# Kernel tuning notes

Hardware: AMD Instinct MI355X
Metric: run time of the kernel (lower is better)

The kernel has to match this reference:

```python
import jax, jax.numpy as jnp
import numpy as np

HIDDEN = 512
B, H, W = 8, 48, 48
SCALE = 1.0 / np.sqrt(HIDDEN).astype(np.float32)


def conv1x1(x, w, b):
    # x: [B, C, H, W], w: [O, C], b: [O]  (1x1 Conv2d == channel matmul)
    return jnp.einsum('bchw,oc->bohw', x, w) + b[None, :, None, None]


def setup_inputs() -> dict:
    key = jax.random.key(0)
    ks = jax.random.split(key, 10)
    s = 1.0 / np.sqrt(HIDDEN)
    return {
        'locx': jax.random.normal(ks[0], (B, HIDDEN, H, W), dtype=jnp.float32),
        'glox': jax.random.normal(ks[1], (B, HIDDEN, H, W), dtype=jnp.float32),
        'Wq': jax.random.normal(ks[2], (HIDDEN, HIDDEN), dtype=jnp.float32) * s,
        'bq': jax.random.normal(ks[3], (HIDDEN,), dtype=jnp.float32) * 0.01,
        'Wk': jax.random.normal(ks[4], (HIDDEN, HIDDEN), dtype=jnp.float32) * s,
        'bk': jax.random.normal(ks[5], (HIDDEN,), dtype=jnp.float32) * 0.01,
        'Wv': jax.random.normal(ks[6], (HIDDEN, HIDDEN), dtype=jnp.float32) * s,
        'bv': jax.random.normal(ks[7], (HIDDEN,), dtype=jnp.float32) * 0.01,
        'Wo': jax.random.normal(ks[8], (HIDDEN, HIDDEN), dtype=jnp.float32) * s,
        'bo': jax.random.normal(ks[9], (HIDDEN,), dtype=jnp.float32) * 0.01,
    }


def reference(locx, glox, Wq, bq, Wk, bk, Wv, bv, Wo, bo):
    b, c, h, w = locx.shape
    # 1x1 conv projections
    q = conv1x1(locx, Wq, bq).reshape(b, c, h * w)   # [B, C, N]
    k = conv1x1(glox, Wk, bk).reshape(b, c, -1)      # [B, C, M]
    v = conv1x1(glox, Wv, bv).reshape(b, c, -1)      # [B, C, M]
    # scores = Q^T K / sqrt(hidden)  -> [B, N, M]
    scores = jnp.einsum('bcn,bcm->bnm', q, k) * SCALE
    probs = jax.nn.softmax(scores, axis=-1)           # dropout rate 0.0 -> identity
    # context = probs @ V^T -> [B, N, C] -> [B, C, H, H]
    ctx = jnp.einsum('bnm,bcm->bcn', probs, v).reshape(b, c, h, h)
    out = conv1x1(ctx, Wo, bo)                        # proj dropout 0.0 -> identity
    return out
```

## Files before the change

kernel.cpp:

```cpp
#include <hip/hip_runtime.h>
#include <hip/hip_bf16.h>

typedef __attribute__((ext_vector_type(4))) float f32x4;
typedef __attribute__((ext_vector_type(8))) short bf16x8;
typedef __attribute__((ext_vector_type(4))) short s16x4;

#define C_DIM 512
#define N_PIX 2304
#define N_BATCH 8
#define ATT_SCALE 0.04419417382415922f
#define NJB 18

typedef __attribute__((address_space(3))) unsigned int lds_u32;
typedef const __attribute__((address_space(1))) unsigned int glob_u32;

__device__ __forceinline__ void gl2lds16(const __hip_bfloat16* g, __hip_bfloat16* l)
{
    __builtin_amdgcn_global_load_lds((glob_u32*)g, (lds_u32*)l, 16, 0, 0);
}

template<int OUT_BF16, int BIAS_MODE, int EPI>
__global__ __launch_bounds__(256)
void gemm_bt(const __hip_bfloat16* __restrict__ A, const __hip_bfloat16* __restrict__ B,
             void* __restrict__ Dp, const float* __restrict__ bias,
             float* __restrict__ rsum,
             float scale, int K, int lda, int ldb, int ldd,
             long sA, long sB, long sD)
{
    __shared__ __hip_bfloat16 As[128 * 64];
    __shared__ __hip_bfloat16 Bs[128 * 64];

    const int tid  = threadIdx.x;
    const int lane = tid & 63;
    const int wave = tid >> 6;
    const int i0 = blockIdx.x * 128;
    const int j0 = blockIdx.y * 128;
    const size_t bz = blockIdx.z;

    const __hip_bfloat16* Ab = A + bz * (size_t)sA;
    const __hip_bfloat16* Bb = B + bz * (size_t)sB;
    __hip_bfloat16* D16 = (__hip_bfloat16*)Dp + bz * (size_t)sD;
    float*          D32 = (float*)Dp          + bz * (size_t)sD;

    const int lrow = lane >> 3;
    const int lcs  = (lane & 7) ^ lrow;
    const __hip_bfloat16* ga = Ab + (size_t)(i0 + wave * 32 + lrow) * lda + lcs * 8;
    const __hip_bfloat16* gb = Bb + (size_t)(j0 + wave * 32 + lrow) * ldb + lcs * 8;
    __hip_bfloat16* la = As + wave * 32 * 64;
    __hip_bfloat16* lb = Bs + wave * 32 * 64;

    const int fr = lane & 15;
    const int fq = lane >> 4;
    const int sw = fr & 7;
    const int wi = (wave >> 1) * 64;
    const int wj = (wave & 1) * 64;

    f32x4 acc[4][4];
#pragma unroll
    for (int a = 0; a < 4; ++a)
#pragma unroll
        for (int b = 0; b < 4; ++b)
            acc[a][b] = (f32x4){0.f, 0.f, 0.f, 0.f};

    for (int k0 = 0; k0 < K; k0 += 64) {
#pragma unroll
        for (int s = 0; s < 4; ++s) {
            gl2lds16(ga + (size_t)s * 8 * lda + k0, la + s * 8 * 64);
            gl2lds16(gb + (size_t)s * 8 * ldb + k0, lb + s * 8 * 64);
        }
        __syncthreads();

#pragma unroll
        for (int kk = 0; kk < 2; ++kk) {
            bf16x8 af[4], bfr[4];
            const int ca = ((kk * 4 + fq) ^ sw) << 3;
#pragma unroll
            for (int t = 0; t < 4; ++t) {
                af[t]  = *(const bf16x8*)(&As[(wi + t * 16 + fr) * 64 + ca]);
                bfr[t] = *(const bf16x8*)(&Bs[(wj + t * 16 + fr) * 64 + ca]);
            }
#pragma unroll
            for (int a = 0; a < 4; ++a)
#pragma unroll
                for (int b = 0; b < 4; ++b)
                    acc[a][b] = __builtin_amdgcn_mfma_f32_16x16x32_bf16(
                        af[a], bfr[b], acc[a][b], 0, 0, 0);
        }
        __syncthreads();
    }

    const int orow = fq * 4;

    float inv[4][4];
    if (EPI == 2) {
        const float* ri = rsum + bz * N_PIX;
#pragma unroll
        for (int a = 0; a < 4; ++a)
#pragma unroll
            for (int r = 0; r < 4; ++r)
                inv[a][r] = ri[i0 + wi + a * 16 + orow + r];
    }

    float rpart[4][4];
    if (EPI == 1) {
#pragma unroll
        for (int a = 0; a < 4; ++a)
#pragma unroll
            for (int r = 0; r < 4; ++r)
                rpart[a][r] = 0.f;
    }

#pragma unroll
    for (int a = 0; a < 4; ++a) {
        int ib = i0 + wi + a * 16 + orow;
#pragma unroll
        for (int b = 0; b < 4; ++b) {
            int j = j0 + wj + b * 16 + fr;
            float bj = (BIAS_MODE == 2) ? bias[j] : 0.f;
#pragma unroll
            for (int r = 0; r < 4; ++r) {
                int i = ib + r;
                float v = acc[a][b][r] * scale;
                if (BIAS_MODE == 1) v += bias[i];
                if (BIAS_MODE == 2) v += bj;
                if (EPI == 1) { v = __expf(v); rpart[a][r] += v; }
                if (EPI == 2) v *= inv[a][r];
                if (OUT_BF16)
                    D16[(size_t)i * ldd + j] = __float2bfloat16(v);
                else
                    D32[(size_t)i * ldd + j] = v;
            }
        }
    }

    if (EPI == 1) {
#pragma unroll
        for (int m = 1; m < 16; m <<= 1)
#pragma unroll
            for (int a = 0; a < 4; ++a)
#pragma unroll
                for (int r = 0; r < 4; ++r)
                    rpart[a][r] += __shfl_xor(rpart[a][r], m);
        float* rsl = (float*)As;
        if (fr == 0) {
#pragma unroll
            for (int a = 0; a < 4; ++a)
#pragma unroll
                for (int r = 0; r < 4; ++r)
                    rsl[wave * 64 + a * 16 + orow + r] = rpart[a][r];
        }
        __syncthreads();
        if (tid < 128) {
            int half = tid >> 6, rr = tid & 63;
            float s = rsl[(half * 2) * 64 + rr] + rsl[(half * 2 + 1) * 64 + rr];
            rsum[((size_t)blockIdx.y * N_BATCH + bz) * N_PIX + i0 + tid] = s;
        }
    }
}

__global__ __launch_bounds__(256)
void reduce_rinv(const float* __restrict__ rp, float* __restrict__ rinv)
{
    int idx = blockIdx.x * 256 + threadIdx.x;
    float s = 0.f;
#pragma unroll
    for (int jb = 0; jb < NJB; ++jb)
        s += rp[(size_t)jb * N_BATCH * N_PIX + idx];
    rinv[idx] = 1.f / s;
}

__global__ __launch_bounds__(256)
void transpose_cast(const float* __restrict__ X, __hip_bfloat16* __restrict__ Xt)
{
    __shared__ float t[64 * 65];
    const int n0 = blockIdx.x * 64;
    const int c0 = blockIdx.y * 64;
    const size_t b = blockIdx.z;
    const float* Xb = X + b * (size_t)C_DIM * N_PIX;
    const int tid = threadIdx.x;

    const int n_l = tid & 63;
    const int c_b = tid >> 6;
#pragma unroll
    for (int s = 0; s < 16; ++s) {
        int c_l = c_b + s * 4;
        t[c_l * 65 + n_l] = Xb[(size_t)(c0 + c_l) * N_PIX + n0 + n_l];
    }
    __syncthreads();

    const int cc = (tid & 7) * 8;
    const int nb = tid >> 3;
#pragma unroll
    for (int it = 0; it < 2; ++it) {
        int n2 = nb + it * 32;
        union { __hip_bfloat16 h[8]; int4 v; } u;
#pragma unroll
        for (int w = 0; w < 8; ++w)
            u.h[w] = __float2bfloat16(t[(cc + w) * 65 + n2]);
        *(int4*)(&Xt[((size_t)b * N_PIX + n0 + n2) * C_DIM + c0 + cc]) = u.v;
    }
}

__global__ __launch_bounds__(256)
void cast_w4(const float* __restrict__ s0, const float* __restrict__ s1,
             const float* __restrict__ s2, const float* __restrict__ s3,
             __hip_bfloat16* __restrict__ dst)
{
    const float* srcs[4] = {s0, s1, s2, s3};
    const int w = blockIdx.y;
    const int i = (blockIdx.x * 256 + threadIdx.x) * 4;
    float4 f = *(const float4*)(srcs[w] + i);
    union { __hip_bfloat16 h[4]; s16x4 q; } t;
    t.h[0] = __float2bfloat16(f.x);
    t.h[1] = __float2bfloat16(f.y);
    t.h[2] = __float2bfloat16(f.z);
    t.h[3] = __float2bfloat16(f.w);
    *(s16x4*)(dst + (size_t)w * C_DIM * C_DIM + i) = t.q;
}

extern "C" void kernel_launch(void* const* d_in, const int* in_sizes, int n_in,
                              void* d_out, int out_size, void* d_ws, size_t ws_size,
                              hipStream_t stream)
{
    const float* locx = (const float*)d_in[0];
    const float* glox = (const float*)d_in[1];
    const float* Wq = (const float*)d_in[2];
    const float* bq = (const float*)d_in[3];
    const float* Wk = (const float*)d_in[4];
    const float* bk = (const float*)d_in[5];
    const float* Wv = (const float*)d_in[6];
    const float* bv = (const float*)d_in[7];
    const float* Wo = (const float*)d_in[8];
    const float* bo = (const float*)d_in[9];
    float* out = (float*)d_out;

    const int C = C_DIM, N = N_PIX;
    const size_t WB   = (size_t)C * C * 2;
    const size_t szX  = (size_t)N_BATCH * N * C * 2;
    const size_t szP1 = (size_t)N * N * 2;
    const size_t szRP = (size_t)NJB * N_BATCH * N * 4;
    const size_t szRI = (size_t)N_BATCH * N * 4;

    const size_t fixed = 4 * WB + 6 * szX + szRP + szRI;
    int nb = 1;
    for (int cand : {8, 4, 2, 1})
        if (ws_size >= fixed + (size_t)cand * szP1 + 8 * 256) { nb = cand; break; }

    char* ws = (char*)d_ws;
    size_t off = 0;
    auto alloc = [&](size_t bytes) {
        char* p = ws + off;
        off += (bytes + 255) & ~(size_t)255;
        return p;
    };
    __hip_bfloat16* wgt = (__hip_bfloat16*)alloc(4 * WB);
    __hip_bfloat16* Xl  = (__hip_bfloat16*)alloc(szX);
    __hip_bfloat16* Xg  = (__hip_bfloat16*)alloc(szX);
    __hip_bfloat16* Qt  = (__hip_bfloat16*)alloc(szX);
    __hip_bfloat16* Kt  = (__hip_bfloat16*)alloc(szX);
    __hip_bfloat16* Vb  = (__hip_bfloat16*)alloc(szX);
    __hip_bfloat16* Ctx = (__hip_bfloat16*)alloc(szX);
    float*          rp   = (float*)alloc(szRP);
    float*          rinv = (float*)alloc(szRI);
    __hip_bfloat16* Pu  = (__hip_bfloat16*)alloc((size_t)nb * szP1);

    __hip_bfloat16* wq_b = wgt;
    __hip_bfloat16* wk_b = wgt + (size_t)C * C;
    __hip_bfloat16* wv_b = wgt + 2 * (size_t)C * C;
    __hip_bfloat16* wo_b = wgt + 3 * (size_t)C * C;

    const dim3 blk(256);
    const long sPr = (long)N * C;
    const long sV  = (long)C * N;

    cast_w4<<<dim3(C * C / 1024, 4), blk, 0, stream>>>(Wq, Wk, Wv, Wo, wgt);
    transpose_cast<<<dim3(N / 64, C / 64, 8), blk, 0, stream>>>(locx, Xl);
    transpose_cast<<<dim3(N / 64, C / 64, 8), blk, 0, stream>>>(glox, Xg);

    gemm_bt<1, 2, 0><<<dim3(N / 128, C / 128, 8), blk, 0, stream>>>(
        Xl, wq_b, Qt, bq, nullptr, 1.f, C, C, C, C, sPr, 0, sPr);
    gemm_bt<1, 2, 0><<<dim3(N / 128, C / 128, 8), blk, 0, stream>>>(
        Xg, wk_b, Kt, bk, nullptr, 1.f, C, C, C, C, sPr, 0, sPr);
    gemm_bt<1, 1, 0><<<dim3(C / 128, N / 128, 8), blk, 0, stream>>>(
        wv_b, Xg, Vb, bv, nullptr, 1.f, C, C, C, N, 0, sPr, sV);

    for (int r = 0; r < N_BATCH; r += nb) {
        gemm_bt<1, 0, 1><<<dim3(N / 128, N / 128, nb), blk, 0, stream>>>(
            Qt + (size_t)r * sPr, Kt + (size_t)r * sPr, Pu, nullptr,
            rp + (size_t)r * N, ATT_SCALE, C, C, C, N, sPr, sPr, (long)N * N);
        reduce_rinv<<<dim3(nb * N / 256), blk, 0, stream>>>(
            rp + (size_t)r * N, rinv + (size_t)r * N);
        gemm_bt<1, 0, 2><<<dim3(N / 128, C / 128, nb), blk, 0, stream>>>(
            Pu, Vb + (size_t)r * sV, Ctx + (size_t)r * sPr, nullptr,
            rinv + (size_t)r * N, 1.f, N, N, N, C, (long)N * N, sV, sPr);
    }

    gemm_bt<0, 1, 0><<<dim3(C / 128, N / 128, 8), blk, 0, stream>>>(
        wo_b, Ctx, out, bo, nullptr, 1.f, C, C, C, N, 0, sPr, sV);
}
```

Before: 390.6 us.

## Remap GEMM grid to batch-fastest 1D order and merge Q/K projections

Replaces the 3D grid with a 1D launch in which the batch index varies fastest, so consecutive workgroups share the same weight tile and reuse it from cache. The Q and K projection GEMMs are merged into one launch that selects operand pointers per block, cutting one kernel launch and raising occupancy on the small projection grids. The workspace fallback is simplified to either all batches at once or one batch at a time. This adds per-block index arithmetic and branching.

```diff
diff --git a/kernel.cpp b/kernel.cpp
--- a/kernel.cpp
+++ b/kernel.cpp
@@ -19,28 +19,41 @@
     __builtin_amdgcn_global_load_lds((glob_u32*)g, (lds_u32*)l, 16, 0, 0);
 }
 
-template<int OUT_BF16, int BIAS_MODE, int EPI>
+template<int OUT_BF16, int BIAS_MODE, int EPI, int MERGE2, int NJ, int NS>
 __global__ __launch_bounds__(256)
-void gemm_bt(const __hip_bfloat16* __restrict__ A, const __hip_bfloat16* __restrict__ B,
-             void* __restrict__ Dp, const float* __restrict__ bias,
+void gemm_bt(const __hip_bfloat16* __restrict__ A0, const __hip_bfloat16* __restrict__ B0,
+             void* __restrict__ D0, const float* __restrict__ bias0,
              float* __restrict__ rsum,
+             const __hip_bfloat16* __restrict__ A1, const __hip_bfloat16* __restrict__ B1,
+             void* __restrict__ D1, const float* __restrict__ bias1,
              float scale, int K, int lda, int ldb, int ldd,
              long sA, long sB, long sD)
 {
     __shared__ __hip_bfloat16 As[128 * 64];
     __shared__ __hip_bfloat16 Bs[128 * 64];
+
+    const int lin = blockIdx.x;
+    const int s   = lin % NS;
+    const int t   = lin / NS;
+    const int bz  = MERGE2 ? (s & 7) : s;
+    const int jb  = t % NJ;
+    const int j0  = jb * 128;
+    const int i0  = (t / NJ) * 128;
+
+    const __hip_bfloat16* A = A0;
+    const __hip_bfloat16* B = B0;
+    void* Dp = (void*)D0;
+    const float* bias = bias0;
+    if (MERGE2 && (s >> 3)) { A = A1; B = B1; Dp = D1; bias = bias1; }
 
     const int tid  = threadIdx.x;
     const int lane = tid & 63;
     const int wave = tid >> 6;
-    const int i0 = blockIdx.x * 128;
-    const int j0 = blockIdx.y * 128;
-    const size_t bz = blockIdx.z;
-
-    const __hip_bfloat16* Ab = A + bz * (size_t)sA;
-    const __hip_bfloat16* Bb = B + bz * (size_t)sB;
-    __hip_bfloat16* D16 = (__hip_bfloat16*)Dp + bz * (size_t)sD;
-    float*          D32 = (float*)Dp          + bz * (size_t)sD;
+
+    const __hip_bfloat16* Ab = A + (size_t)bz * (size_t)sA;
+    const __hip_bfloat16* Bb = B + (size_t)bz * (size_t)sB;
+    __hip_bfloat16* D16 = (__hip_bfloat16*)Dp + (size_t)bz * (size_t)sD;
+    float*          D32 = (float*)Dp          + (size_t)bz * (size_t)sD;
 
     const int lrow = lane >> 3;
     const int lcs  = (lane & 7) ^ lrow;
@@ -64,9 +77,9 @@
 
     for (int k0 = 0; k0 < K; k0 += 64) {
 #pragma unroll
-        for (int s = 0; s < 4; ++s) {
-            gl2lds16(ga + (size_t)s * 8 * lda + k0, la + s * 8 * 64);
-            gl2lds16(gb + (size_t)s * 8 * ldb + k0, lb + s * 8 * 64);
+        for (int ss = 0; ss < 4; ++ss) {
+            gl2lds16(ga + (size_t)ss * 8 * lda + k0, la + ss * 8 * 64);
+            gl2lds16(gb + (size_t)ss * 8 * ldb + k0, lb + ss * 8 * 64);
         }
         __syncthreads();
 
@@ -75,9 +88,9 @@
             bf16x8 af[4], bfr[4];
             const int ca = ((kk * 4 + fq) ^ sw) << 3;
 #pragma unroll
-            for (int t = 0; t < 4; ++t) {
-                af[t]  = *(const bf16x8*)(&As[(wi + t * 16 + fr) * 64 + ca]);
-                bfr[t] = *(const bf16x8*)(&Bs[(wj + t * 16 + fr) * 64 + ca]);
+            for (int tt = 0; tt < 4; ++tt) {
+                af[tt]  = *(const bf16x8*)(&As[(wi + tt * 16 + fr) * 64 + ca]);
+                bfr[tt] = *(const bf16x8*)(&Bs[(wj + tt * 16 + fr) * 64 + ca]);
             }
 #pragma unroll
             for (int a = 0; a < 4; ++a)
@@ -93,7 +106,7 @@
 
     float inv[4][4];
     if (EPI == 2) {
-        const float* ri = rsum + bz * N_PIX;
+        const float* ri = rsum + (size_t)bz * N_PIX;
 #pragma unroll
         for (int a = 0; a < 4; ++a)
 #pragma unroll
@@ -152,8 +165,8 @@
         __syncthreads();
         if (tid < 128) {
             int half = tid >> 6, rr = tid & 63;
-            float s = rsl[(half * 2) * 64 + rr] + rsl[(half * 2 + 1) * 64 + rr];
-            rsum[((size_t)blockIdx.y * N_BATCH + bz) * N_PIX + i0 + tid] = s;
+            float sm = rsl[(half * 2) * 64 + rr] + rsl[(half * 2 + 1) * 64 + rr];
+            rsum[((size_t)jb * N_BATCH + bz) * N_PIX + i0 + tid] = sm;
         }
     }
 }
@@ -242,9 +255,7 @@
     const size_t szRI = (size_t)N_BATCH * N * 4;
 
     const size_t fixed = 4 * WB + 6 * szX + szRP + szRI;
-    int nb = 1;
-    for (int cand : {8, 4, 2, 1})
-        if (ws_size >= fixed + (size_t)cand * szP1 + 8 * 256) { nb = cand; break; }
+    bool full = (ws_size >= fixed + 8 * szP1 + 8 * 256);
 
     char* ws = (char*)d_ws;
     size_t off = 0;
@@ -262,7 +273,7 @@
     __hip_bfloat16* Ctx = (__hip_bfloat16*)alloc(szX);
     float*          rp   = (float*)alloc(szRP);
     float*          rinv = (float*)alloc(szRI);
-    __hip_bfloat16* Pu  = (__hip_bfloat16*)alloc((size_t)nb * szP1);
+    __hip_bfloat16* Pu  = (__hip_bfloat16*)alloc(full ? 8 * szP1 : szP1);
 
     __hip_bfloat16* wq_b = wgt;
     __hip_bfloat16* wk_b = wgt + (size_t)C * C;
@@ -277,24 +288,37 @@
     transpose_cast<<<dim3(N / 64, C / 64, 8), blk, 0, stream>>>(locx, Xl);
     transpose_cast<<<dim3(N / 64, C / 64, 8), blk, 0, stream>>>(glox, Xg);
 
-    gemm_bt<1, 2, 0><<<dim3(N / 128, C / 128, 8), blk, 0, stream>>>(
-        Xl, wq_b, Qt, bq, nullptr, 1.f, C, C, C, C, sPr, 0, sPr);
-    gemm_bt<1, 2, 0><<<dim3(N / 128, C / 128, 8), blk, 0, stream>>>(
-        Xg, wk_b, Kt, bk, nullptr, 1.f, C, C, C, C, sPr, 0, sPr);
-    gemm_bt<1, 1, 0><<<dim3(C / 128, N / 128, 8), blk, 0, stream>>>(
-        wv_b, Xg, Vb, bv, nullptr, 1.f, C, C, C, N, 0, sPr, sV);
-
-    for (int r = 0; r < N_BATCH; r += nb) {
-        gemm_bt<1, 0, 1><<<dim3(N / 128, N / 128, nb), blk, 0, stream>>>(
-            Qt + (size_t)r * sPr, Kt + (size_t)r * sPr, Pu, nullptr,
-            rp + (size_t)r * N, ATT_SCALE, C, C, C, N, sPr, sPr, (long)N * N);
-        reduce_rinv<<<dim3(nb * N / 256), blk, 0, stream>>>(
-            rp + (size_t)r * N, rinv + (size_t)r * N);
-        gemm_bt<1, 0, 2><<<dim3(N / 128, C / 128, nb), blk, 0, stream>>>(
-            Pu, Vb + (size_t)r * sV, Ctx + (size_t)r * sPr, nullptr,
-            rinv + (size_t)r * N, 1.f, N, N, N, C, (long)N * N, sV, sPr);
-    }
-
-    gemm_bt<0, 1, 0><<<dim3(C / 128, N / 128, 8), blk, 0, stream>>>(
-        wo_b, Ctx, out, bo, nullptr, 1.f, C, C, C, N, 0, sPr, sV);
-}
+    gemm_bt<1, 2, 0, 1, 4, 16><<<dim3(18 * 4 * 16), blk, 0, stream>>>(
+        Xl, wq_b, Qt, bq, nullptr, Xg, wk_b, Kt, bk,
+        1.f, C, C, C, C, sPr, 0, sPr);
+    gemm_bt<1, 1, 0, 0, 18, 8><<<dim3(4 * 18 * 8), blk, 0, stream>>>(
+        wv_b, Xg, Vb, bv, nullptr, nullptr, nullptr, nullptr, nullptr,
+        1.f, C, C, C, N, 0, sPr, sV);
+
+    if (full) {
+        gemm_bt<1, 0, 1, 0, 18, 8><<<dim3(18 * 18 * 8), blk, 0, stream>>>(
+            Qt, Kt, Pu, nullptr, rp, nullptr, nullptr, nullptr, nullptr,
+            ATT_SCALE, C, C, C, N, sPr, sPr, (long)N * N);
+        reduce_rinv<<<dim3(8 * N / 256), blk, 0, stream>>>(rp, rinv);
+        gemm_bt<1, 0, 2, 0, 4, 8><<<dim3(18 * 4 * 8), blk, 0, stream>>>(
+            Pu, Vb, Ctx, nullptr, rinv, nullptr, nullptr, nullptr, nullptr,
+            1.f, N, N, N, C, (long)N * N, sV, sPr);
+    } else {
+        for (int r = 0; r < N_BATCH; ++r) {
+            gemm_bt<1, 0, 1, 0, 18, 1><<<dim3(18 * 18), blk, 0, stream>>>(
+                Qt + (size_t)r * sPr, Kt + (size_t)r * sPr, Pu, nullptr,
+                rp + (size_t)r * N, nullptr, nullptr, nullptr, nullptr,
+                ATT_SCALE, C, C, C, N, 0, 0, 0);
+            reduce_rinv<<<dim3(N / 256), blk, 0, stream>>>(
+                rp + (size_t)r * N, rinv + (size_t)r * N);
+            gemm_bt<1, 0, 2, 0, 4, 1><<<dim3(18 * 4), blk, 0, stream>>>(
+                Pu, Vb + (size_t)r * sV, Ctx + (size_t)r * sPr, nullptr,
+                rinv + (size_t)r * N, nullptr, nullptr, nullptr, nullptr,
+                1.f, N, N, N, C, 0, 0, 0);
+        }
+    }
+
+    gemm_bt<0, 1, 0, 0, 18, 8><<<dim3(4 * 18 * 8), blk, 0, stream>>>(
+        wo_b, Ctx, out, bo, nullptr, nullptr, nullptr, nullptr, nullptr,
+        1.f, C, C, C, N, 0, sPr, (long)C * N);
+}
```

Result: faster. 368.2 us (-5.7%).
